# Kernel tuning notes

Measured on AMD Instinct MI355X. Metric: run time of the kernel, lower is better.

The kernel has to match this reference:

```python
import jax, jax.numpy as jnp
import numpy as np

NUM_NODES = 65536       # B * gcn_nodes_num = 256 * 256
NODES_PER_GRAPH = 256
GCN_EMB_DIM = 128
N_EMBD = 512
NUM_EDGES = 1048576     # avg degree 16
NEG_SLOPE = 0.1


def gcn_conv(x, edge_index, W, b, num_nodes):
    """PyG GCNConv: add self-loops, symmetric normalization, linear, aggregate."""
    loop = jnp.arange(num_nodes, dtype=edge_index.dtype)
    src = jnp.concatenate([edge_index[0], loop])
    dst = jnp.concatenate([edge_index[1], loop])
    deg = jax.ops.segment_sum(jnp.ones_like(dst, dtype=x.dtype), dst,
                              num_segments=num_nodes)
    dinv = jnp.where(deg > 0, jax.lax.rsqrt(deg), jnp.zeros_like(deg))
    norm = dinv[src] * dinv[dst]              # [E+N]
    h = x @ W                                 # [N, out]
    msg = h[src] * norm[:, None]              # [E+N, out]
    out = jax.ops.segment_sum(msg, dst, num_segments=num_nodes)
    return out + b


def setup_inputs() -> dict:
    key = jax.random.key(0)
    ks = jax.random.split(key, 8)
    nodes = jax.random.normal(ks[0], (NUM_NODES, 3), dtype=jnp.float32)
    edge_index = jax.random.randint(ks[1], (2, NUM_EDGES), 0, NUM_NODES,
                                    dtype=jnp.int64)
    W1 = jax.random.normal(ks[2], (3, 3), dtype=jnp.float32) * 0.5
    b1 = jnp.zeros((3,), dtype=jnp.float32)
    W2 = jax.random.normal(ks[3], (3, GCN_EMB_DIM), dtype=jnp.float32) * 0.5
    b2 = jnp.zeros((GCN_EMB_DIM,), dtype=jnp.float32)
    W3 = jax.random.normal(ks[4], (GCN_EMB_DIM * NODES_PER_GRAPH, N_EMBD),
                           dtype=jnp.float32) * 0.01
    b3 = jnp.zeros((N_EMBD,), dtype=jnp.float32)
    return {"nodes": nodes, "edge_index": edge_index,
            "W1": W1, "b1": b1, "W2": W2, "b2": b2, "W3": W3, "b3": b3}


def reference(nodes, edge_index, W1, b1, W2, b2, W3, b3):
    n = nodes.shape[0]
    h = gcn_conv(nodes, edge_index, W1, b1, n)           # GCNConv(3,3)
    h = jnp.where(h >= 0, h, NEG_SLOPE * h)              # leaky_relu(0.1)
    h = gcn_conv(h, edge_index, W2, b2, n)               # GCNConv(3,128)
    h = h.reshape(-1, GCN_EMB_DIM * NODES_PER_GRAPH)     # [B, 128*256]
    out = h @ W3 + b3                                    # [B, 512]
    return out
```

## Files before the change

### kernel.cpp

```cpp
#include <hip/hip_runtime.h>

static constexpr int NN   = 65536;
static constexpr int NPG  = 256;
static constexpr int NB   = 256;
static constexpr int EMB  = 128;
static constexpr int NOUT = 512;

static constexpr int NBIN = 256;
static constexpr int CAP  = 4608;
static constexpr int VBLK = 128;

static constexpr int BT = 8;
static constexpr int KS = 16;
static constexpr int IC = NPG / KS;

__global__ __launch_bounds__(1024)
void k_partV(const int* __restrict__ src, const int* __restrict__ dst, int E,
             int* __restrict__ gbin, int* __restrict__ part,
             const float* __restrict__ W2, const float* __restrict__ b2,
             const float* __restrict__ W3, float* __restrict__ V) {
    int tid = threadIdx.x;
    int bid = blockIdx.x;
    if (bid >= NBIN) {
        int vb = bid - NBIN;
        int i = vb * 2 + (tid >> 9);
        int j = tid & 511;
        float acc0 = 0.f, acc1 = 0.f, acc2 = 0.f, acc3 = 0.f;
        const float* w3 = W3 + (size_t)i * EMB * NOUT + j;
        for (int c = 0; c < EMB; c++) {
            float v = w3[(size_t)c * NOUT];
            acc0 += W2[0*EMB+c] * v;
            acc1 += W2[1*EMB+c] * v;
            acc2 += W2[2*EMB+c] * v;
            acc3 += b2[c]       * v;
        }
        float* o = V + (size_t)i * 4 * NOUT + j;
        o[0*NOUT] = acc0; o[1*NOUT] = acc1; o[2*NOUT] = acc2; o[3*NOUT] = acc3;
        return;
    }
    __shared__ int hist[NBIN], loff[NBIN], base[NBIN], scanbuf[NBIN];
    __shared__ int stage[4096];
    int epb = (E + NBIN - 1) / NBIN;
    int e0 = bid * epb;
    int e1 = min(e0 + epb, E);
    if (tid < NBIN) hist[tid] = 0;
    __syncthreads();

    int pk[4], bn[4], rk[4];
    int n = 0;
    int e = e0 + tid * 4;
    if (e + 4 <= e1) {
        int4 s4 = *(const int4*)(src + e);
        int4 d4 = *(const int4*)(dst + e);
        int ss[4] = {s4.x, s4.y, s4.z, s4.w};
        int dd[4] = {d4.x, d4.y, d4.z, d4.w};
#pragma unroll
        for (int k = 0; k < 4; k++) {
            pk[k] = ss[k] | ((dd[k] & 255) << 16);
            bn[k] = dd[k] >> 8;
            rk[k] = atomicAdd(&hist[bn[k]], 1);
        }
        n = 4;
    } else {
        for (int k = 0; k < 4 && e + k < e1; k++) {
            int s = src[e+k], d = dst[e+k];
            pk[n] = s | ((d & 255) << 16);
            bn[n] = d >> 8;
            rk[n] = atomicAdd(&hist[bn[n]], 1);
            n++;
        }
    }
    __syncthreads();

    if (tid < NBIN) scanbuf[tid] = hist[tid];
    __syncthreads();
    for (int off = 1; off < NBIN; off <<= 1) {
        int v = 0;
        if (tid < NBIN && tid >= off) v = scanbuf[tid - off];
        __syncthreads();
        if (tid < NBIN) scanbuf[tid] += v;
        __syncthreads();
    }
    if (tid < NBIN) {
        loff[tid] = scanbuf[tid] - hist[tid];
        base[tid] = atomicAdd(&gbin[tid], hist[tid]);
    }
    __syncthreads();

    for (int k = 0; k < n; k++) stage[loff[bn[k]] + rk[k]] = pk[k];
    __syncthreads();

    int bin = tid >> 2;
    int cnt = hist[bin], bs = base[bin], lo = loff[bin];
    for (int t = tid & 3; t < cnt; t += 4) {
        int gp = bs + t;
        if (gp < CAP) part[bin * CAP + gp] = stage[lo + t];
    }
}

__global__ void k_csr(const int* __restrict__ gbin, const int* __restrict__ part,
                      const float* __restrict__ nodes,
                      float* __restrict__ dinv, float4* __restrict__ y1,
                      int* __restrict__ rs, unsigned short* __restrict__ srt) {
    __shared__ int pkst[CAP];
    __shared__ int hist[NPG], scanb[NPG], off_[NPG];
    __shared__ unsigned short stageS[CAP];
    int tid = threadIdx.x, bin = blockIdx.x;
    hist[tid] = 0;
    __syncthreads();
    int cnt = min(gbin[bin], CAP);
    const int* pp = part + (size_t)bin * CAP;
    for (int e = tid; e < cnt; e += 256) {
        int p = pp[e];
        pkst[e] = p;
        atomicAdd(&hist[(p >> 16) & 255], 1);
    }
    __syncthreads();
    scanb[tid] = hist[tid];
    __syncthreads();
    for (int off = 1; off < NPG; off <<= 1) {
        int v = (tid >= off) ? scanb[tid - off] : 0;
        __syncthreads();
        scanb[tid] += v;
        __syncthreads();
    }
    int start = scanb[tid] - hist[tid];
    off_[tid] = start;
    int node = bin * NPG + tid;
    float di = rsqrtf((float)(hist[tid] + 1));
    dinv[node] = di;
    y1[node] = make_float4(nodes[3*node+0] * di, nodes[3*node+1] * di,
                           nodes[3*node+2] * di, 0.f);
    rs[node] = start | (hist[tid] << 20);
    __syncthreads();
    for (int e = tid; e < cnt; e += 256) {
        int p = pkst[e];
        int pos = atomicAdd(&off_[(p >> 16) & 255], 1);
        stageS[pos] = (unsigned short)(p & 0xFFFF);
    }
    __syncthreads();
    const unsigned int* so = (const unsigned int*)stageS;
    unsigned int* g = (unsigned int*)(srt + (size_t)bin * CAP);
    for (int t = tid; t < (cnt + 1) >> 1; t += 256) g[t] = so[t];
}

__global__ void k_agg1(const int* __restrict__ rs, const unsigned short* __restrict__ srt,
                       const float* __restrict__ dinv, const float4* __restrict__ y1,
                       const float* __restrict__ W1, const float* __restrict__ b1,
                       float4* __restrict__ y2) {
    int gid = blockIdx.x * 256 + threadIdx.x;
    int i = gid >> 2, sub = gid & 3;
    int rsd = rs[i];
    int start = rsd & 0xFFFFF, deg = rsd >> 20;
    const unsigned short* sp = srt + (size_t)(i >> 8) * CAP + start;
    float ax = 0.f, ay = 0.f, az = 0.f;
    for (int k = sub; k < deg; k += 4) {
        float4 v = y1[sp[k]];
        ax += v.x; ay += v.y; az += v.z;
    }
    ax += __shfl_xor(ax, 1); ay += __shfl_xor(ay, 1); az += __shfl_xor(az, 1);
    ax += __shfl_xor(ax, 2); ay += __shfl_xor(ay, 2); az += __shfl_xor(az, 2);
    if (sub == 0) {
        float4 self = y1[i];
        float di = dinv[i];
        float a0 = (ax + self.x) * di, a1 = (ay + self.y) * di, a2 = (az + self.z) * di;
        float h[3];
#pragma unroll
        for (int k = 0; k < 3; k++) {
            float t = a0 * W1[0*3+k] + a1 * W1[1*3+k] + a2 * W1[2*3+k] + b1[k];
            t = (t >= 0.f) ? t : 0.1f * t;
            h[k] = t * di;
        }
        y2[i] = make_float4(h[0], h[1], h[2], 0.f);
    }
}

__global__ void k_agg2(const int* __restrict__ rs, const unsigned short* __restrict__ srt,
                       const float* __restrict__ dinv, const float4* __restrict__ y2,
                       float4* __restrict__ agg2) {
    int gid = blockIdx.x * 256 + threadIdx.x;
    int i = gid >> 2, sub = gid & 3;
    int rsd = rs[i];
    int start = rsd & 0xFFFFF, deg = rsd >> 20;
    const unsigned short* sp = srt + (size_t)(i >> 8) * CAP + start;
    float ax = 0.f, ay = 0.f, az = 0.f;
    for (int k = sub; k < deg; k += 4) {
        float4 v = y2[sp[k]];
        ax += v.x; ay += v.y; az += v.z;
    }
    ax += __shfl_xor(ax, 1); ay += __shfl_xor(ay, 1); az += __shfl_xor(az, 1);
    ax += __shfl_xor(ax, 2); ay += __shfl_xor(ay, 2); az += __shfl_xor(az, 2);
    if (sub == 0) {
        float4 self = y2[i];
        float di = dinv[i];
        agg2[i] = make_float4((ax + self.x) * di, (ay + self.y) * di,
                              (az + self.z) * di, 0.f);
    }
}

__global__ void k_out_part(const float4* __restrict__ agg2, const float* __restrict__ V,
                           float* __restrict__ part) {
    __shared__ float4 a_s[BT * IC];
    int tid = threadIdx.x;
    int j  = blockIdx.x * 256 + tid;
    int b0 = blockIdx.y * BT;
    int i0 = blockIdx.z * IC;
    for (int idx = tid; idx < BT * IC; idx += 256) {
        int t = idx / IC, i = idx % IC;
        a_s[idx] = agg2[(size_t)(b0 + t) * NPG + i0 + i];
    }
    __syncthreads();

    float acc[BT];
#pragma unroll
    for (int t = 0; t < BT; t++) acc[t] = 0.f;

    const float* vj = V + (size_t)i0 * 4 * NOUT + j;
    for (int i = 0; i < IC; i++) {
        float v0 = vj[(size_t)(i*4+0) * NOUT];
        float v1 = vj[(size_t)(i*4+1) * NOUT];
        float v2 = vj[(size_t)(i*4+2) * NOUT];
        float v3 = vj[(size_t)(i*4+3) * NOUT];
#pragma unroll
        for (int t = 0; t < BT; t++) {
            float4 a = a_s[t*IC + i];
            acc[t] += a.x * v0 + a.y * v1 + a.z * v2 + v3;
        }
    }
#pragma unroll
    for (int t = 0; t < BT; t++)
        part[((size_t)blockIdx.z * NB + b0 + t) * NOUT + j] = acc[t];
}

__global__ void k_reduce(const float* __restrict__ part, const float* __restrict__ b3,
                         float* __restrict__ out) {
    int idx = blockIdx.x * 256 + threadIdx.x;
    int j = idx & (NOUT - 1);
    float acc = b3[j];
#pragma unroll
    for (int s = 0; s < KS; s++) acc += part[(size_t)s * NB * NOUT + idx];
    out[idx] = acc;
}

extern "C" void kernel_launch(void* const* d_in, const int* in_sizes, int n_in,
                              void* d_out, int out_size, void* d_ws, size_t ws_size,
                              hipStream_t stream) {
    const float* nodes = (const float*)d_in[0];
    const int*   ei    = (const int*)  d_in[1];
    const float* W1    = (const float*)d_in[2];
    const float* b1    = (const float*)d_in[3];
    const float* W2    = (const float*)d_in[4];
    const float* b2    = (const float*)d_in[5];
    const float* W3    = (const float*)d_in[6];
    const float* b3    = (const float*)d_in[7];
    float* out = (float*)d_out;

    const int E = in_sizes[1] / 2;
    const int* src = ei;
    const int* dst = ei + E;

    char* ws = (char*)d_ws;
    float4* y1    = (float4*)ws;
    float4* y2    = y1 + NN;
    float4* agg2  = y2 + NN;
    float*  V     = (float*)(agg2 + NN);
    float*  partO = V + (size_t)NPG * 4 * NOUT;
    int*    partE = (int*)(partO + (size_t)KS * NB * NOUT);
    unsigned short* srt = (unsigned short*)(partE + (size_t)NBIN * CAP);
    int*    rs    = (int*)(srt + (size_t)NBIN * CAP);
    float*  dinv  = (float*)(rs + NN);
    int*    gbin  = (int*)(dinv + NN);

    hipMemsetAsync(gbin, 0, NBIN * 4, stream);
    k_partV   <<<NBIN + VBLK, 1024, 0, stream>>>(src, dst, E, gbin, partE, W2, b2, W3, V);
    k_csr     <<<NBIN,  256, 0, stream>>>(gbin, partE, nodes, dinv, y1, rs, srt);
    k_agg1    <<<NN*4/256, 256, 0, stream>>>(rs, srt, dinv, y1, W1, b1, y2);
    k_agg2    <<<NN*4/256, 256, 0, stream>>>(rs, srt, dinv, y2, agg2);
    k_out_part<<<dim3(2, NB/BT, KS), 256, 0, stream>>>(agg2, V, partO);
    k_reduce  <<<NB*NOUT/256,        256, 0, stream>>>(partO, b3, out);
}
```

Measured before the change: 166.8 us.

## Split W3 fold across more blocks, widen aggregation lanes, vectorize V and reduce

The W2·W3 fold now runs one node-slot per block, with the channel loop split into two halves that are combined through shared memory, so it uses 256 blocks instead of 128. V is stored interleaved as float4, letting the output GEMM read it with a single vector load. The CSR build uses 512 threads, aggregation uses 8 lanes per node instead of 4, and the final reduce works on float4. Together these aim for more parallelism and wider memory accesses, at the cost of more shuffle steps and some idle lanes on low-degree nodes.

New measurement: 168.2 us. No clear change (+0.8%).

```diff
diff --git a/kernel.cpp b/kernel.cpp
--- a/kernel.cpp
+++ b/kernel.cpp
@@ -8,7 +8,6 @@
 
 static constexpr int NBIN = 256;
 static constexpr int CAP  = 4608;
-static constexpr int VBLK = 128;
 
 static constexpr int BT = 8;
 static constexpr int KS = 16;
@@ -18,32 +17,49 @@
 void k_partV(const int* __restrict__ src, const int* __restrict__ dst, int E,
              int* __restrict__ gbin, int* __restrict__ part,
              const float* __restrict__ W2, const float* __restrict__ b2,
-             const float* __restrict__ W3, float* __restrict__ V) {
+             const float* __restrict__ W3, float4* __restrict__ V4) {
+    union SH {
+        struct { int hist[NBIN]; int loff[NBIN]; int base[NBIN]; int scanbuf[NBIN];
+                 int stage[4096]; } part;
+        struct { float red[2][4][NOUT]; } bv;
+    };
+    __shared__ SH sh;
     int tid = threadIdx.x;
     int bid = blockIdx.x;
+
     if (bid >= NBIN) {
-        int vb = bid - NBIN;
-        int i = vb * 2 + (tid >> 9);
+        int i = bid - NBIN;
         int j = tid & 511;
-        float acc0 = 0.f, acc1 = 0.f, acc2 = 0.f, acc3 = 0.f;
-        const float* w3 = W3 + (size_t)i * EMB * NOUT + j;
-        for (int c = 0; c < EMB; c++) {
+        int half = tid >> 9;
+        const float* w3 = W3 + (size_t)i * EMB * NOUT + (size_t)half * 64 * NOUT + j;
+        float a0 = 0.f, a1 = 0.f, a2 = 0.f, a3 = 0.f;
+        for (int c = 0; c < 64; c++) {
             float v = w3[(size_t)c * NOUT];
-            acc0 += W2[0*EMB+c] * v;
-            acc1 += W2[1*EMB+c] * v;
-            acc2 += W2[2*EMB+c] * v;
-            acc3 += b2[c]       * v;
-        }
-        float* o = V + (size_t)i * 4 * NOUT + j;
-        o[0*NOUT] = acc0; o[1*NOUT] = acc1; o[2*NOUT] = acc2; o[3*NOUT] = acc3;
+            int cc = half * 64 + c;
+            a0 += W2[0*EMB+cc] * v;
+            a1 += W2[1*EMB+cc] * v;
+            a2 += W2[2*EMB+cc] * v;
+            a3 += b2[cc]       * v;
+        }
+        sh.bv.red[half][0][j] = a0;
+        sh.bv.red[half][1][j] = a1;
+        sh.bv.red[half][2][j] = a2;
+        sh.bv.red[half][3][j] = a3;
+        __syncthreads();
+        if (tid < NOUT) {
+            float4 r;
+            r.x = sh.bv.red[0][0][tid] + sh.bv.red[1][0][tid];
+            r.y = sh.bv.red[0][1][tid] + sh.bv.red[1][1][tid];
+            r.z = sh.bv.red[0][2][tid] + sh.bv.red[1][2][tid];
+            r.w = sh.bv.red[0][3][tid] + sh.bv.red[1][3][tid];
+            V4[(size_t)i * NOUT + tid] = r;
+        }
         return;
     }
-    __shared__ int hist[NBIN], loff[NBIN], base[NBIN], scanbuf[NBIN];
-    __shared__ int stage[4096];
     int epb = (E + NBIN - 1) / NBIN;
     int e0 = bid * epb;
     int e1 = min(e0 + epb, E);
-    if (tid < NBIN) hist[tid] = 0;
+    if (tid < NBIN) sh.part.hist[tid] = 0;
     __syncthreads();
 
     int pk[4], bn[4], rk[4];
@@ -58,7 +74,7 @@
         for (int k = 0; k < 4; k++) {
             pk[k] = ss[k] | ((dd[k] & 255) << 16);
             bn[k] = dd[k] >> 8;
-            rk[k] = atomicAdd(&hist[bn[k]], 1);
+            rk[k] = atomicAdd(&sh.part.hist[bn[k]], 1);
         }
         n = 4;
     } else {
@@ -66,74 +82,78 @@
             int s = src[e+k], d = dst[e+k];
             pk[n] = s | ((d & 255) << 16);
             bn[n] = d >> 8;
-            rk[n] = atomicAdd(&hist[bn[n]], 1);
+            rk[n] = atomicAdd(&sh.part.hist[bn[n]], 1);
             n++;
         }
     }
     __syncthreads();
 
-    if (tid < NBIN) scanbuf[tid] = hist[tid];
+    if (tid < NBIN) sh.part.scanbuf[tid] = sh.part.hist[tid];
     __syncthreads();
     for (int off = 1; off < NBIN; off <<= 1) {
         int v = 0;
-        if (tid < NBIN && tid >= off) v = scanbuf[tid - off];
-        __syncthreads();
-        if (tid < NBIN) scanbuf[tid] += v;
+        if (tid < NBIN && tid >= off) v = sh.part.scanbuf[tid - off];
+        __syncthreads();
+        if (tid < NBIN) sh.part.scanbuf[tid] += v;
         __syncthreads();
     }
     if (tid < NBIN) {
-        loff[tid] = scanbuf[tid] - hist[tid];
-        base[tid] = atomicAdd(&gbin[tid], hist[tid]);
-    }
-    __syncthreads();
-
-    for (int k = 0; k < n; k++) stage[loff[bn[k]] + rk[k]] = pk[k];
+        sh.part.loff[tid] = sh.part.scanbuf[tid] - sh.part.hist[tid];
+        sh.part.base[tid] = atomicAdd(&gbin[tid], sh.part.hist[tid]);
+    }
+    __syncthreads();
+
+    for (int k = 0; k < n; k++) sh.part.stage[sh.part.loff[bn[k]] + rk[k]] = pk[k];
     __syncthreads();
 
     int bin = tid >> 2;
-    int cnt = hist[bin], bs = base[bin], lo = loff[bin];
+    int cnt = sh.part.hist[bin], bs = sh.part.base[bin], lo = sh.part.loff[bin];
     for (int t = tid & 3; t < cnt; t += 4) {
         int gp = bs + t;
-        if (gp < CAP) part[bin * CAP + gp] = stage[lo + t];
-    }
-}
-
-__global__ void k_csr(const int* __restrict__ gbin, const int* __restrict__ part,
-                      const float* __restrict__ nodes,
-                      float* __restrict__ dinv, float4* __restrict__ y1,
-                      int* __restrict__ rs, unsigned short* __restrict__ srt) {
+        if (gp < CAP) part[bin * CAP + gp] = sh.part.stage[lo + t];
+    }
+}
+
+__global__ __launch_bounds__(512)
+void k_csr(const int* __restrict__ gbin, const int* __restrict__ part,
+           const float* __restrict__ nodes,
+           float* __restrict__ dinv, float4* __restrict__ y1,
+           int* __restrict__ rs, unsigned short* __restrict__ srt) {
     __shared__ int pkst[CAP];
     __shared__ int hist[NPG], scanb[NPG], off_[NPG];
     __shared__ unsigned short stageS[CAP];
     int tid = threadIdx.x, bin = blockIdx.x;
-    hist[tid] = 0;
+    if (tid < NPG) hist[tid] = 0;
     __syncthreads();
     int cnt = min(gbin[bin], CAP);
     const int* pp = part + (size_t)bin * CAP;
-    for (int e = tid; e < cnt; e += 256) {
+    for (int e = tid; e < cnt; e += 512) {
         int p = pp[e];
         pkst[e] = p;
         atomicAdd(&hist[(p >> 16) & 255], 1);
     }
     __syncthreads();
-    scanb[tid] = hist[tid];
+    if (tid < NPG) scanb[tid] = hist[tid];
     __syncthreads();
     for (int off = 1; off < NPG; off <<= 1) {
-        int v = (tid >= off) ? scanb[tid - off] : 0;
-        __syncthreads();
-        scanb[tid] += v;
-        __syncthreads();
-    }
-    int start = scanb[tid] - hist[tid];
-    off_[tid] = start;
-    int node = bin * NPG + tid;
-    float di = rsqrtf((float)(hist[tid] + 1));
-    dinv[node] = di;
-    y1[node] = make_float4(nodes[3*node+0] * di, nodes[3*node+1] * di,
-                           nodes[3*node+2] * di, 0.f);
-    rs[node] = start | (hist[tid] << 20);
-    __syncthreads();
-    for (int e = tid; e < cnt; e += 256) {
+        int v = 0;
+        if (tid < NPG && tid >= off) v = scanb[tid - off];
+        __syncthreads();
+        if (tid < NPG) scanb[tid] += v;
+        __syncthreads();
+    }
+    if (tid < NPG) {
+        int start = scanb[tid] - hist[tid];
+        off_[tid] = start;
+        int node = bin * NPG + tid;
+        float di = rsqrtf((float)(hist[tid] + 1));
+        dinv[node] = di;
+        y1[node] = make_float4(nodes[3*node+0] * di, nodes[3*node+1] * di,
+                               nodes[3*node+2] * di, 0.f);
+        rs[node] = start | (hist[tid] << 20);
+    }
+    __syncthreads();
+    for (int e = tid; e < cnt; e += 512) {
         int p = pkst[e];
         int pos = atomicAdd(&off_[(p >> 16) & 255], 1);
         stageS[pos] = (unsigned short)(p & 0xFFFF);
@@ -141,64 +161,62 @@
     __syncthreads();
     const unsigned int* so = (const unsigned int*)stageS;
     unsigned int* g = (unsigned int*)(srt + (size_t)bin * CAP);
-    for (int t = tid; t < (cnt + 1) >> 1; t += 256) g[t] = so[t];
+    for (int t = tid; t < (cnt + 1) >> 1; t += 512) g[t] = so[t];
+}
+
+__device__ __forceinline__ void agg_pass(int g, const int* __restrict__ rs,
+                                         const unsigned short* __restrict__ srt,
+                                         const float* __restrict__ dinv,
+                                         const float* __restrict__ W1,
+                                         const float* __restrict__ b1,
+                                         const float4* __restrict__ yin,
+                                         float4* __restrict__ yout, bool first) {
+    int i = g >> 3, sub = g & 7;
+    int rsd = rs[i];
+    int start = rsd & 0xFFFFF, deg = rsd >> 20;
+    const unsigned short* sp = srt + (size_t)(i >> 8) * CAP + start;
+    float ax = 0.f, ay = 0.f, az = 0.f;
+    for (int k = sub; k < deg; k += 8) {
+        float4 v = yin[sp[k]];
+        ax += v.x; ay += v.y; az += v.z;
+    }
+    ax += __shfl_xor(ax, 1); ay += __shfl_xor(ay, 1); az += __shfl_xor(az, 1);
+    ax += __shfl_xor(ax, 2); ay += __shfl_xor(ay, 2); az += __shfl_xor(az, 2);
+    ax += __shfl_xor(ax, 4); ay += __shfl_xor(ay, 4); az += __shfl_xor(az, 4);
+    if (sub == 0) {
+        float4 self = yin[i];
+        float di = dinv[i];
+        float a0 = (ax + self.x) * di, a1 = (ay + self.y) * di, a2 = (az + self.z) * di;
+        if (first) {
+            float h[3];
+#pragma unroll
+            for (int k = 0; k < 3; k++) {
+                float t = a0 * W1[0*3+k] + a1 * W1[1*3+k] + a2 * W1[2*3+k] + b1[k];
+                t = (t >= 0.f) ? t : 0.1f * t;
+                h[k] = t * di;
+            }
+            yout[i] = make_float4(h[0], h[1], h[2], 0.f);
+        } else {
+            yout[i] = make_float4(a0, a1, a2, 0.f);
+        }
+    }
 }
 
 __global__ void k_agg1(const int* __restrict__ rs, const unsigned short* __restrict__ srt,
                        const float* __restrict__ dinv, const float4* __restrict__ y1,
                        const float* __restrict__ W1, const float* __restrict__ b1,
                        float4* __restrict__ y2) {
-    int gid = blockIdx.x * 256 + threadIdx.x;
-    int i = gid >> 2, sub = gid & 3;
-    int rsd = rs[i];
-    int start = rsd & 0xFFFFF, deg = rsd >> 20;
-    const unsigned short* sp = srt + (size_t)(i >> 8) * CAP + start;
-    float ax = 0.f, ay = 0.f, az = 0.f;
-    for (int k = sub; k < deg; k += 4) {
-        float4 v = y1[sp[k]];
-        ax += v.x; ay += v.y; az += v.z;
-    }
-    ax += __shfl_xor(ax, 1); ay += __shfl_xor(ay, 1); az += __shfl_xor(az, 1);
-    ax += __shfl_xor(ax, 2); ay += __shfl_xor(ay, 2); az += __shfl_xor(az, 2);
-    if (sub == 0) {
-        float4 self = y1[i];
-        float di = dinv[i];
-        float a0 = (ax + self.x) * di, a1 = (ay + self.y) * di, a2 = (az + self.z) * di;
-        float h[3];
-#pragma unroll
-        for (int k = 0; k < 3; k++) {
-            float t = a0 * W1[0*3+k] + a1 * W1[1*3+k] + a2 * W1[2*3+k] + b1[k];
-            t = (t >= 0.f) ? t : 0.1f * t;
-            h[k] = t * di;
-        }
-        y2[i] = make_float4(h[0], h[1], h[2], 0.f);
-    }
+    agg_pass(blockIdx.x * 256 + threadIdx.x, rs, srt, dinv, W1, b1, y1, y2, true);
 }
 
 __global__ void k_agg2(const int* __restrict__ rs, const unsigned short* __restrict__ srt,
                        const float* __restrict__ dinv, const float4* __restrict__ y2,
                        float4* __restrict__ agg2) {
-    int gid = blockIdx.x * 256 + threadIdx.x;
-    int i = gid >> 2, sub = gid & 3;
-    int rsd = rs[i];
-    int start = rsd & 0xFFFFF, deg = rsd >> 20;
-    const unsigned short* sp = srt + (size_t)(i >> 8) * CAP + start;
-    float ax = 0.f, ay = 0.f, az = 0.f;
-    for (int k = sub; k < deg; k += 4) {
-        float4 v = y2[sp[k]];
-        ax += v.x; ay += v.y; az += v.z;
-    }
-    ax += __shfl_xor(ax, 1); ay += __shfl_xor(ay, 1); az += __shfl_xor(az, 1);
-    ax += __shfl_xor(ax, 2); ay += __shfl_xor(ay, 2); az += __shfl_xor(az, 2);
-    if (sub == 0) {
-        float4 self = y2[i];
-        float di = dinv[i];
-        agg2[i] = make_float4((ax + self.x) * di, (ay + self.y) * di,
-                              (az + self.z) * di, 0.f);
-    }
-}
-
-__global__ void k_out_part(const float4* __restrict__ agg2, const float* __restrict__ V,
+    agg_pass(blockIdx.x * 256 + threadIdx.x, rs, srt, dinv, nullptr, nullptr,
+             y2, agg2, false);
+}
+
+__global__ void k_out_part(const float4* __restrict__ agg2, const float4* __restrict__ V4,
                            float* __restrict__ part) {
     __shared__ float4 a_s[BT * IC];
     int tid = threadIdx.x;
@@ -215,16 +233,13 @@
 #pragma unroll
     for (int t = 0; t < BT; t++) acc[t] = 0.f;
 
-    const float* vj = V + (size_t)i0 * 4 * NOUT + j;
+    const float4* vj = V4 + (size_t)i0 * NOUT + j;
     for (int i = 0; i < IC; i++) {
-        float v0 = vj[(size_t)(i*4+0) * NOUT];
-        float v1 = vj[(size_t)(i*4+1) * NOUT];
-        float v2 = vj[(size_t)(i*4+2) * NOUT];
-        float v3 = vj[(size_t)(i*4+3) * NOUT];
+        float4 v = vj[(size_t)i * NOUT];
 #pragma unroll
         for (int t = 0; t < BT; t++) {
             float4 a = a_s[t*IC + i];
-            acc[t] += a.x * v0 + a.y * v1 + a.z * v2 + v3;
+            acc[t] += a.x * v.x + a.y * v.y + a.z * v.z + v.w;
         }
     }
 #pragma unroll
@@ -232,14 +247,17 @@
         part[((size_t)blockIdx.z * NB + b0 + t) * NOUT + j] = acc[t];
 }
 
-__global__ void k_reduce(const float* __restrict__ part, const float* __restrict__ b3,
-                         float* __restrict__ out) {
+__global__ void k_reduce(const float4* __restrict__ part4, const float4* __restrict__ b3_4,
+                         float4* __restrict__ out4) {
     int idx = blockIdx.x * 256 + threadIdx.x;
-    int j = idx & (NOUT - 1);
-    float acc = b3[j];
-#pragma unroll
-    for (int s = 0; s < KS; s++) acc += part[(size_t)s * NB * NOUT + idx];
-    out[idx] = acc;
+    int j4 = idx & (NOUT/4 - 1);
+    float4 acc = b3_4[j4];
+#pragma unroll
+    for (int s = 0; s < KS; s++) {
+        float4 v = part4[(size_t)s * (NB*NOUT/4) + idx];
+        acc.x += v.x; acc.y += v.y; acc.z += v.z; acc.w += v.w;
+    }
+    out4[idx] = acc;
 }
 
 extern "C" void kernel_launch(void* const* d_in, const int* in_sizes, int n_in,
@@ -253,29 +271,29 @@
     const float* b2    = (const float*)d_in[5];
     const float* W3    = (const float*)d_in[6];
     const float* b3    = (const float*)d_in[7];
-    float* out = (float*)d_out;
 
     const int E = in_sizes[1] / 2;
     const int* src = ei;
     const int* dst = ei + E;
 
     char* ws = (char*)d_ws;
-    float4* y1    = (float4*)ws;
+    int*    gbin  = (int*)ws;
+    float4* y1    = (float4*)(ws + 1024);
     float4* y2    = y1 + NN;
     float4* agg2  = y2 + NN;
-    float*  V     = (float*)(agg2 + NN);
-    float*  partO = V + (size_t)NPG * 4 * NOUT;
+    float4* V4    = agg2 + NN;
+    float*  partO = (float*)(V4 + (size_t)NPG * NOUT);
     int*    partE = (int*)(partO + (size_t)KS * NB * NOUT);
     unsigned short* srt = (unsigned short*)(partE + (size_t)NBIN * CAP);
     int*    rs    = (int*)(srt + (size_t)NBIN * CAP);
     float*  dinv  = (float*)(rs + NN);
-    int*    gbin  = (int*)(dinv + NN);
 
     hipMemsetAsync(gbin, 0, NBIN * 4, stream);
-    k_partV   <<<NBIN + VBLK, 1024, 0, stream>>>(src, dst, E, gbin, partE, W2, b2, W3, V);
-    k_csr     <<<NBIN,  256, 0, stream>>>(gbin, partE, nodes, dinv, y1, rs, srt);
-    k_agg1    <<<NN*4/256, 256, 0, stream>>>(rs, srt, dinv, y1, W1, b1, y2);
-    k_agg2    <<<NN*4/256, 256, 0, stream>>>(rs, srt, dinv, y2, agg2);
-    k_out_part<<<dim3(2, NB/BT, KS), 256, 0, stream>>>(agg2, V, partO);
-    k_reduce  <<<NB*NOUT/256,        256, 0, stream>>>(partO, b3, out);
-}
+    k_partV   <<<2*NBIN, 1024, 0, stream>>>(src, dst, E, gbin, partE, W2, b2, W3, V4);
+    k_csr     <<<NBIN,    512, 0, stream>>>(gbin, partE, nodes, dinv, y1, rs, srt);
+    k_agg1    <<<NN*8/256, 256, 0, stream>>>(rs, srt, dinv, y1, W1, b1, y2);
+    k_agg2    <<<NN*8/256, 256, 0, stream>>>(rs, srt, dinv, y2, agg2);
+    k_out_part<<<dim3(2, NB/BT, KS), 256, 0, stream>>>(agg2, V4, partO);
+    k_reduce  <<<NB*NOUT/4/256,      256, 0, stream>>>((const float4*)partO,
+                                                       (const float4*)b3, (float4*)d_out);
+}
```
